# Kernel tuning notes

Hardware: AMD Instinct MI355X
Metric: run time of the kernel (lower is better)

## Reference

```python
import jax, jax.numpy as jnp
import numpy as np

H = 256
V_IN = 32000
V_OUT = 32000
T = 2048


def setup_inputs() -> dict:
    key = jax.random.key(0)
    ks = jax.random.split(key, 16)
    s = 1.0 / np.sqrt(H)
    inp = {
        "src": jax.random.randint(ks[0], (T, 1), 0, V_IN, dtype=jnp.int64 if jax.config.jax_enable_x64 else jnp.int32),
        "trg": jax.random.randint(ks[1], (T, 1), 0, V_OUT, dtype=jnp.int64 if jax.config.jax_enable_x64 else jnp.int32),
        "enc_emb": jax.random.normal(ks[2], (V_IN, H), jnp.float32),
        "enc_W_ih": jax.random.uniform(ks[3], (3 * H, H), jnp.float32, -s, s),
        "enc_W_hh": jax.random.uniform(ks[4], (3 * H, H), jnp.float32, -s, s),
        "enc_b_ih": jax.random.uniform(ks[5], (3 * H,), jnp.float32, -s, s),
        "enc_b_hh": jax.random.uniform(ks[6], (3 * H,), jnp.float32, -s, s),
        "dec_emb": jax.random.normal(ks[7], (V_OUT, H), jnp.float32),
        "dec_W_ih": jax.random.uniform(ks[8], (3 * H, H), jnp.float32, -s, s),
        "dec_W_hh": jax.random.uniform(ks[9], (3 * H, H), jnp.float32, -s, s),
        "dec_b_ih": jax.random.uniform(ks[10], (3 * H,), jnp.float32, -s, s),
        "dec_b_hh": jax.random.uniform(ks[11], (3 * H,), jnp.float32, -s, s),
        "out_W": jax.random.uniform(ks[12], (V_OUT, H), jnp.float32, -s, s),
        "out_b": jax.random.uniform(ks[13], (V_OUT,), jnp.float32, -s, s),
    }
    return inp


def _gru_step(x, h, W_ih, W_hh, b_ih, b_hh):
    # PyTorch GRU cell math. x,h: [H]
    gi = W_ih @ x + b_ih          # [3H]
    gh = W_hh @ h + b_hh          # [3H]
    i_r, i_z, i_n = jnp.split(gi, 3)
    h_r, h_z, h_n = jnp.split(gh, 3)
    r = jax.nn.sigmoid(i_r + h_r)
    z = jax.nn.sigmoid(i_z + h_z)
    n = jnp.tanh(i_n + r * h_n)
    return (1.0 - z) * n + z * h


def reference(src, trg, enc_emb, enc_W_ih, enc_W_hh, enc_b_ih, enc_b_hh,
              dec_emb, dec_W_ih, dec_W_hh, dec_b_ih, dec_b_hh, out_W, out_b):
    src_t = src[:, 0]  # [T], batch forced to 1 by .view(1,1,-1)
    trg_t = trg[:, 0]  # [T]
    h0 = jnp.zeros((H,), enc_emb.dtype)

    def step(h, toks):
        s_tok, t_tok = toks
        # encoder step
        h = _gru_step(enc_emb[s_tok], h, enc_W_ih, enc_W_hh, enc_b_ih, enc_b_hh)
        # decoder step (relu on embedding per source)
        x_d = jax.nn.relu(dec_emb[t_tok])
        h = _gru_step(x_d, h, dec_W_ih, dec_W_hh, dec_b_ih, dec_b_hh)
        logits = out_W @ h + out_b          # [V_OUT]
        return h, jax.nn.log_softmax(logits)

    _, outs = jax.lax.scan(step, h0, (src_t, trg_t))
    return outs[:, None, :]  # [T, 1, V_OUT]
```

## Files before the change

kernel.cpp:

```cpp
#include <hip/hip_runtime.h>
#include <hip/hip_bf16.h>

#define T_STEPS 2048
#define HDIM 256
#define VOUT 32000

typedef short short8 __attribute__((ext_vector_type(8)));
typedef float f32x4 __attribute__((ext_vector_type(4)));

#if defined(__has_builtin)
#if __has_builtin(__builtin_amdgcn_sdot4)
#define HAVE_SDOT4 1
#endif
#if __has_builtin(__builtin_amdgcn_mov_dpp)
#define HAVE_DPP 1
#endif
#if __has_builtin(__builtin_amdgcn_rcpf)
#define HAVE_RCP 1
#endif
#endif

__device__ __forceinline__ int dot4i8(int a, int b, int c) {
#ifdef HAVE_SDOT4
    return __builtin_amdgcn_sdot4(a, b, c, false);
#else
#pragma unroll
    for (int k = 0; k < 4; ++k) {
        int av = (a << (24 - 8 * k)) >> 24;
        int bv = (b << (24 - 8 * k)) >> 24;
        c += av * bv;
    }
    return c;
#endif
}

__device__ __forceinline__ int pairsum(int x) {
#ifdef HAVE_DPP
    return x + __builtin_amdgcn_mov_dpp(x, 0xB1, 0xF, 0xF, true);
#else
    return x + __shfl_xor(x, 1);
#endif
}

__device__ __forceinline__ float fast_rcp(float x) {
#ifdef HAVE_RCP
    return __builtin_amdgcn_rcpf(x);
#else
    return 1.0f / x;
#endif
}

__device__ __forceinline__ float fast_sigmoid(float x) {
    return fast_rcp(1.0f + __expf(-x));
}
__device__ __forceinline__ float fast_tanh(float x) {
    float ax = fabsf(x);
    float e = __expf(-2.0f * ax);
    float t = 1.0f - 2.0f * e * fast_rcp(1.0f + e);
    return copysignf(t, x);
}

__global__ void k_quant(const float* __restrict__ W, int* __restrict__ wq,
                        float* __restrict__ sc) {
    int row = blockIdx.x;
    int t = threadIdx.x;
    float4 w = ((const float4*)(W + (size_t)row * HDIM))[t];
    float m = fmaxf(fmaxf(fabsf(w.x), fabsf(w.y)), fmaxf(fabsf(w.z), fabsf(w.w)));
#pragma unroll
    for (int off = 32; off; off >>= 1) m = fmaxf(m, __shfl_xor(m, off));
    float inv = (m > 0.0f) ? 127.0f / m : 0.0f;
    float scale = (m > 0.0f) ? m * (1.0f / 127.0f) : 0.0f;
    int q0 = __float2int_rn(w.x * inv); q0 = max(-127, min(127, q0));
    int q1 = __float2int_rn(w.y * inv); q1 = max(-127, min(127, q1));
    int q2 = __float2int_rn(w.z * inv); q2 = max(-127, min(127, q2));
    int q3 = __float2int_rn(w.w * inv); q3 = max(-127, min(127, q3));
    int packed = (q0 & 255) | ((q1 & 255) << 8) | ((q2 & 255) << 16) | ((q3 & 255) << 24);
    wq[row * 64 + t] = packed;
    if (t == 0) sc[row] = scale;
}

__global__ __launch_bounds__(256) void k_cvt(const float* __restrict__ in,
                                             unsigned short* __restrict__ out, int n4) {
    int i = blockIdx.x * 256 + threadIdx.x;
    if (i < n4) {
        float4 v = ((const float4*)in)[i];
        unsigned int u[4] = {__float_as_uint(v.x), __float_as_uint(v.y),
                             __float_as_uint(v.z), __float_as_uint(v.w)};
        ushort4 o;
        o.x = (unsigned short)((u[0] + 0x7FFFu + ((u[0] >> 16) & 1)) >> 16);
        o.y = (unsigned short)((u[1] + 0x7FFFu + ((u[1] >> 16) & 1)) >> 16);
        o.z = (unsigned short)((u[2] + 0x7FFFu + ((u[2] >> 16) & 1)) >> 16);
        o.w = (unsigned short)((u[3] + 0x7FFFu + ((u[3] >> 16) & 1)) >> 16);
        ((ushort4*)out)[i] = o;
    }
}

__global__ __launch_bounds__(256) void k_gi(const int* __restrict__ toks,
                                            const float* __restrict__ emb,
                                            const float* __restrict__ W,
                                            const float* __restrict__ b,
                                            float* __restrict__ gi, int do_relu) {
    __shared__ float4 xs[64];
    int t = blockIdx.x;
    int tid = threadIdx.x;
    int tok = toks[t];
    if (tid < 64) {
        float4 x = ((const float4*)(emb + (size_t)tok * HDIM))[tid];
        if (do_relu) {
            x.x = fmaxf(x.x, 0.0f); x.y = fmaxf(x.y, 0.0f);
            x.z = fmaxf(x.z, 0.0f); x.w = fmaxf(x.w, 0.0f);
        }
        xs[tid] = x;
    }
    __syncthreads();
#pragma unroll
    for (int g = 0; g < 3; ++g) {
        int row = tid + g * 256;
        const float4* wr = (const float4*)(W + (size_t)row * HDIM);
        float acc = b[row];
#pragma unroll 16
        for (int k = 0; k < 64; ++k) {
            float4 w = wr[k];
            float4 x = xs[k];
            acc += w.x * x.x + w.y * x.y + w.z * x.z + w.w * x.w;
        }
        gi[(size_t)t * 768 + row] = acc;
    }
}

__global__ __launch_bounds__(512, 2) void k_gru(
    const int* __restrict__ wq_e, const float* __restrict__ sc_e,
    const float* __restrict__ bhh_e, const float* __restrict__ gi_e,
    const int* __restrict__ wq_d, const float* __restrict__ sc_d,
    const float* __restrict__ bhh_d, const float* __restrict__ gi_d,
    unsigned short* __restrict__ h_bf) {
    __shared__ __align__(16) int HQA[64];
    __shared__ __align__(16) int HQB[64];

    const int tid = threadIdx.x;
    const int rg = tid >> 1;
    const int c  = tid & 1;

    int we[3][32], wd[3][32];
    float se[3], sd[3], be[3], bd[3];
#pragma unroll
    for (int j = 0; j < 3; ++j) {
        const int row = rg + j * 256;
        const int4* pe = (const int4*)(wq_e + (row * 64 + c * 32));
        const int4* pd = (const int4*)(wq_d + (row * 64 + c * 32));
#pragma unroll
        for (int i = 0; i < 8; ++i) {
            int4 a = pe[i];
            we[j][4 * i + 0] = a.x; we[j][4 * i + 1] = a.y;
            we[j][4 * i + 2] = a.z; we[j][4 * i + 3] = a.w;
            int4 bq = pd[i];
            wd[j][4 * i + 0] = bq.x; wd[j][4 * i + 1] = bq.y;
            wd[j][4 * i + 2] = bq.z; wd[j][4 * i + 3] = bq.w;
        }
        se[j] = sc_e[row] * (1.0f / 127.0f);
        sd[j] = sc_d[row] * (1.0f / 127.0f);
        be[j] = bhh_e[row];
        bd[j] = bhh_d[row];
    }

    float h = 0.0f;
    if (tid < 64) HQA[tid] = 0;
    __syncthreads();

    const float* ge = gi_e + rg;
    const float* gd = gi_d + rg;
    unsigned short* hop = h_bf + rg;

    float eg0 = ge[0], eg1 = ge[256], eg2 = ge[512];

    for (int t = 0; t < T_STEPS; ++t) {
        float dg0 = gd[0], dg1 = gd[256], dg2 = gd[512];
        gd += 768;

        {
            const int4* hq4 = ((const int4*)HQA) + c * 8;
            int p0 = 0, p1 = 0, p2 = 0;
#pragma unroll
            for (int i = 0; i < 8; ++i) {
                int4 v = hq4[i];
                p0 = dot4i8(we[0][4 * i + 0], v.x, p0);
                p1 = dot4i8(we[1][4 * i + 0], v.x, p1);
                p2 = dot4i8(we[2][4 * i + 0], v.x, p2);
                p0 = dot4i8(we[0][4 * i + 1], v.y, p0);
                p1 = dot4i8(we[1][4 * i + 1], v.y, p1);
                p2 = dot4i8(we[2][4 * i + 1], v.y, p2);
                p0 = dot4i8(we[0][4 * i + 2], v.z, p0);
                p1 = dot4i8(we[1][4 * i + 2], v.z, p1);
                p2 = dot4i8(we[2][4 * i + 2], v.z, p2);
                p0 = dot4i8(we[0][4 * i + 3], v.w, p0);
                p1 = dot4i8(we[1][4 * i + 3], v.w, p1);
                p2 = dot4i8(we[2][4 * i + 3], v.w, p2);
            }
            int f0 = pairsum(p0), f1 = pairsum(p1), f2 = pairsum(p2);
            float r = fast_sigmoid(eg0 + se[0] * (float)f0 + be[0]);
            float z = fast_sigmoid(eg1 + se[1] * (float)f1 + be[1]);
            float n = fast_tanh(eg2 + r * (se[2] * (float)f2 + be[2]));
            h = (1.0f - z) * n + z * h;
            if (c == 0)
                ((signed char*)HQB)[rg] = (signed char)__float2int_rn(h * 127.0f);
        }
        __syncthreads();

        {
            const float* gen = (t < T_STEPS - 1) ? (ge + 768) : (gi_e + rg);
            eg0 = gen[0]; eg1 = gen[256]; eg2 = gen[512];
            ge = gen;
        }

        {
            const int4* hq4 = ((const int4*)HQB) + c * 8;
            int p0 = 0, p1 = 0, p2 = 0;
#pragma unroll
            for (int i = 0; i < 8; ++i) {
                int4 v = hq4[i];
                p0 = dot4i8(wd[0][4 * i + 0], v.x, p0);
                p1 = dot4i8(wd[1][4 * i + 0], v.x, p1);
                p2 = dot4i8(wd[2][4 * i + 0], v.x, p2);
                p0 = dot4i8(wd[0][4 * i + 1], v.y, p0);
                p1 = dot4i8(wd[1][4 * i + 1], v.y, p1);
                p2 = dot4i8(wd[2][4 * i + 1], v.y, p2);
                p0 = dot4i8(wd[0][4 * i + 2], v.z, p0);
                p1 = dot4i8(wd[1][4 * i + 2], v.z, p1);
                p2 = dot4i8(wd[2][4 * i + 2], v.z, p2);
                p0 = dot4i8(wd[0][4 * i + 3], v.w, p0);
                p1 = dot4i8(wd[1][4 * i + 3], v.w, p1);
                p2 = dot4i8(wd[2][4 * i + 3], v.w, p2);
            }
            int f0 = pairsum(p0), f1 = pairsum(p1), f2 = pairsum(p2);
            float r = fast_sigmoid(dg0 + sd[0] * (float)f0 + bd[0]);
            float z = fast_sigmoid(dg1 + sd[1] * (float)f1 + bd[1]);
            float n = fast_tanh(dg2 + r * (sd[2] * (float)f2 + bd[2]));
            h = (1.0f - z) * n + z * h;
            if (c == 0) {
                ((signed char*)HQA)[rg] = (signed char)__float2int_rn(h * 127.0f);
                unsigned int u = __float_as_uint(h);
                *hop = (unsigned short)((u + 0x7FFFu + ((u >> 16) & 1)) >> 16);
            }
            hop += 256;
        }
        __syncthreads();
    }
}

__global__ __launch_bounds__(256) void k_logits(const unsigned short* __restrict__ hb,
                                                const unsigned short* __restrict__ wb,
                                                const float* __restrict__ out_b,
                                                float* __restrict__ out) {
    const int vb = blockIdx.x * 64;
    const int tb = blockIdx.y * 64;
    const int w = threadIdx.x >> 6;
    const int l = threadIdx.x & 63;
    const int m = l & 15;
    const int q = l >> 4;

    const unsigned short* aptr = hb + (size_t)(tb + w * 16 + m) * HDIM + q * 8;
    const unsigned short* bptr = wb + (size_t)(vb + m) * HDIM + q * 8;

    short8 af[8];
#pragma unroll
    for (int kt = 0; kt < 8; ++kt) af[kt] = *(const short8*)(aptr + kt * 32);

    f32x4 acc[4];
#pragma unroll
    for (int nt = 0; nt < 4; ++nt)
#pragma unroll
        for (int r = 0; r < 4; ++r) acc[nt][r] = 0.0f;

#pragma unroll
    for (int nt = 0; nt < 4; ++nt) {
        const unsigned short* bp = bptr + (size_t)nt * 16 * HDIM;
#pragma unroll
        for (int kt = 0; kt < 8; ++kt) {
            short8 bf = *(const short8*)(bp + kt * 32);
            acc[nt] = __builtin_amdgcn_mfma_f32_16x16x32_bf16(af[kt], bf, acc[nt], 0, 0, 0);
        }
    }
#pragma unroll
    for (int nt = 0; nt < 4; ++nt) {
        float bias = out_b[vb + nt * 16 + m];
#pragma unroll
        for (int r = 0; r < 4; ++r) {
            out[(size_t)(tb + w * 16 + q * 4 + r) * VOUT + vb + nt * 16 + m] =
                acc[nt][r] + bias;
        }
    }
}

__global__ __launch_bounds__(256) void k_lsesub(float* __restrict__ out) {
    const int t = blockIdx.x;
    const int tid = threadIdx.x;
    float* rowp = out + (size_t)t * VOUT;
    float m = -3.0e38f, l = 0.0f;
    for (int v = tid; v < VOUT; v += 256) {
        float x = rowp[v];
        float M = fmaxf(m, x);
        l = l * __expf(m - M) + __expf(x - M);
        m = M;
    }
#pragma unroll
    for (int off = 32; off; off >>= 1) {
        float m2 = __shfl_xor(m, off);
        float l2 = __shfl_xor(l, off);
        float M = fmaxf(m, m2);
        l = l * __expf(m - M) + l2 * __expf(m2 - M);
        m = M;
    }
    __shared__ float sm[4], sl[4];
    __shared__ float s_lse;
    int lane = tid & 63, wv = tid >> 6;
    if (lane == 0) { sm[wv] = m; sl[wv] = l; }
    __syncthreads();
    if (tid == 0) {
        float M = fmaxf(fmaxf(sm[0], sm[1]), fmaxf(sm[2], sm[3]));
        float L = sl[0] * __expf(sm[0] - M) + sl[1] * __expf(sm[1] - M) +
                  sl[2] * __expf(sm[2] - M) + sl[3] * __expf(sm[3] - M);
        s_lse = M + __logf(L);
    }
    __syncthreads();
    float s = s_lse;
    float4* p4 = (float4*)rowp;
    for (int i = tid; i < VOUT / 4; i += 256) {
        float4 o = p4[i];
        o.x -= s; o.y -= s; o.z -= s; o.w -= s;
        p4[i] = o;
    }
}

extern "C" void kernel_launch(void* const* d_in, const int* in_sizes, int n_in,
                              void* d_out, int out_size, void* d_ws, size_t ws_size,
                              hipStream_t stream) {
    (void)in_sizes; (void)n_in; (void)out_size; (void)ws_size;
    const int*   src      = (const int*)d_in[0];
    const int*   trg      = (const int*)d_in[1];
    const float* enc_emb  = (const float*)d_in[2];
    const float* enc_W_ih = (const float*)d_in[3];
    const float* enc_W_hh = (const float*)d_in[4];
    const float* enc_b_ih = (const float*)d_in[5];
    const float* enc_b_hh = (const float*)d_in[6];
    const float* dec_emb  = (const float*)d_in[7];
    const float* dec_W_ih = (const float*)d_in[8];
    const float* dec_W_hh = (const float*)d_in[9];
    const float* dec_b_ih = (const float*)d_in[10];
    const float* dec_b_hh = (const float*)d_in[11];
    const float* out_W    = (const float*)d_in[12];
    const float* out_b    = (const float*)d_in[13];
    float* out = (float*)d_out;

    char* ws = (char*)d_ws;
    float* gi_e  = (float*)ws; ws += (size_t)T_STEPS * 768 * 4;
    float* gi_d  = (float*)ws; ws += (size_t)T_STEPS * 768 * 4;
    float* sc_e  = (float*)ws; ws += 768 * 4;
    float* sc_d  = (float*)ws; ws += 768 * 4;
    int*   wq_e  = (int*)ws;   ws += 768 * 64 * 4;
    int*   wq_d  = (int*)ws;   ws += 768 * 64 * 4;
    unsigned short* h_bf = (unsigned short*)ws; ws += (size_t)T_STEPS * HDIM * 2;
    unsigned short* w_bf = (unsigned short*)ws; ws += (size_t)VOUT * HDIM * 2;

    k_quant<<<768, 64, 0, stream>>>(enc_W_hh, wq_e, sc_e);
    k_quant<<<768, 64, 0, stream>>>(dec_W_hh, wq_d, sc_d);
    k_cvt<<<(VOUT * HDIM / 4 + 255) / 256, 256, 0, stream>>>(out_W, w_bf, VOUT * HDIM / 4);
    k_gi<<<T_STEPS, 256, 0, stream>>>(src, enc_emb, enc_W_ih, enc_b_ih, gi_e, 0);
    k_gi<<<T_STEPS, 256, 0, stream>>>(trg, dec_emb, dec_W_ih, dec_b_ih, gi_d, 1);
    k_gru<<<1, 512, 0, stream>>>(wq_e, sc_e, enc_b_hh, gi_e,
                                 wq_d, sc_d, dec_b_hh, gi_d, h_bf);
    k_logits<<<dim3(VOUT / 64, T_STEPS / 64), 256, 0, stream>>>(h_bf, w_bf, out_b, out);
    k_lsesub<<<T_STEPS, 256, 0, stream>>>(out);
}
```

Before: 3.783 ms.

## Split GRU recurrence across four lanes per row pair with DPP butterfly reduction

The sequential GRU kernel now assigns two hidden units to each group of four lanes, and each lane computes a quarter-K slice for both units. A two-stage DPP exchange (xor1 swap-add, then xor2) reduces the partial sums, so each step runs half as many serial dot4 operations per lane on the critical path. The r and z hidden biases are folded into the precomputed input gates, and __syncthreads is replaced with an explicit lgkmcnt wait plus s_barrier. The cost is more cross-lane shuffles and a changed register layout, held under a waves_per_eu attribute.

```diff
diff --git a/kernel.cpp b/kernel.cpp
--- a/kernel.cpp
+++ b/kernel.cpp
@@ -34,11 +34,18 @@
 #endif
 }
 
-__device__ __forceinline__ int pairsum(int x) {
+__device__ __forceinline__ int xor1_add(int keep, int send) {
 #ifdef HAVE_DPP
-    return x + __builtin_amdgcn_mov_dpp(x, 0xB1, 0xF, 0xF, true);
+    return keep + __builtin_amdgcn_mov_dpp(send, 0xB1, 0xF, 0xF, true);
 #else
-    return x + __shfl_xor(x, 1);
+    return keep + __shfl_xor(send, 1);
+#endif
+}
+__device__ __forceinline__ int xor2_sum(int x) {
+#ifdef HAVE_DPP
+    return x + __builtin_amdgcn_mov_dpp(x, 0x4E, 0xF, 0xF, true);
+#else
+    return x + __shfl_xor(x, 2);
 #endif
 }
 
@@ -49,7 +56,6 @@
     return 1.0f / x;
 #endif
 }
-
 __device__ __forceinline__ float fast_sigmoid(float x) {
     return fast_rcp(1.0f + __expf(-x));
 }
@@ -58,6 +64,10 @@
     float e = __expf(-2.0f * ax);
     float t = 1.0f - 2.0f * e * fast_rcp(1.0f + e);
     return copysignf(t, x);
+}
+
+__device__ __forceinline__ void barrier_lds() {
+    asm volatile("s_waitcnt lgkmcnt(0)\n\ts_barrier" ::: "memory");
 }
 
 __global__ void k_quant(const float* __restrict__ W, int* __restrict__ wq,
@@ -99,6 +109,7 @@
                                             const float* __restrict__ emb,
                                             const float* __restrict__ W,
                                             const float* __restrict__ b,
+                                            const float* __restrict__ bhh,
                                             float* __restrict__ gi, int do_relu) {
     __shared__ float4 xs[64];
     int t = blockIdx.x;
@@ -117,7 +128,7 @@
     for (int g = 0; g < 3; ++g) {
         int row = tid + g * 256;
         const float4* wr = (const float4*)(W + (size_t)row * HDIM);
-        float acc = b[row];
+        float acc = b[row] + ((g < 2) ? bhh[row] : 0.0f);
 #pragma unroll 16
         for (int k = 0; k < 64; ++k) {
             float4 w = wr[k];
@@ -128,7 +139,8 @@
     }
 }
 
-__global__ __launch_bounds__(512, 2) void k_gru(
+__global__ __launch_bounds__(512)
+__attribute__((amdgpu_waves_per_eu(2, 2))) void k_gru(
     const int* __restrict__ wq_e, const float* __restrict__ sc_e,
     const float* __restrict__ bhh_e, const float* __restrict__ gi_e,
     const int* __restrict__ wq_d, const float* __restrict__ sc_d,
@@ -138,38 +150,47 @@
     __shared__ __align__(16) int HQB[64];
 
     const int tid = threadIdx.x;
-    const int rg = tid >> 1;
-    const int c  = tid & 1;
-
-    int we[3][32], wd[3][32];
-    float se[3], sd[3], be[3], bd[3];
-#pragma unroll
-    for (int j = 0; j < 3; ++j) {
-        const int row = rg + j * 256;
-        const int4* pe = (const int4*)(wq_e + (row * 64 + c * 32));
-        const int4* pd = (const int4*)(wq_d + (row * 64 + c * 32));
-#pragma unroll
-        for (int i = 0; i < 8; ++i) {
-            int4 a = pe[i];
-            we[j][4 * i + 0] = a.x; we[j][4 * i + 1] = a.y;
-            we[j][4 * i + 2] = a.z; we[j][4 * i + 3] = a.w;
-            int4 bq = pd[i];
-            wd[j][4 * i + 0] = bq.x; wd[j][4 * i + 1] = bq.y;
-            wd[j][4 * i + 2] = bq.z; wd[j][4 * i + 3] = bq.w;
-        }
-        se[j] = sc_e[row] * (1.0f / 127.0f);
-        sd[j] = sc_d[row] * (1.0f / 127.0f);
-        be[j] = bhh_e[row];
-        bd[j] = bhh_d[row];
-    }
+    const int q  = tid >> 2;
+    const int c  = tid & 3;
+    const int el = c & 1;
+    const int e  = 2 * q + el;
+    const bool wr = (c & 2) == 0;
+
+    int we[6][16], wd[6][16];
+#pragma unroll
+    for (int eo = 0; eo < 2; ++eo) {
+#pragma unroll
+        for (int g = 0; g < 3; ++g) {
+            const int row = 2 * q + eo + 256 * g;
+            const int4* pe = (const int4*)(wq_e + (row * 64 + c * 16));
+            const int4* pd = (const int4*)(wq_d + (row * 64 + c * 16));
+#pragma unroll
+            for (int i = 0; i < 4; ++i) {
+                int4 a = pe[i];
+                we[eo * 3 + g][4 * i + 0] = a.x; we[eo * 3 + g][4 * i + 1] = a.y;
+                we[eo * 3 + g][4 * i + 2] = a.z; we[eo * 3 + g][4 * i + 3] = a.w;
+                int4 bq = pd[i];
+                wd[eo * 3 + g][4 * i + 0] = bq.x; wd[eo * 3 + g][4 * i + 1] = bq.y;
+                wd[eo * 3 + g][4 * i + 2] = bq.z; wd[eo * 3 + g][4 * i + 3] = bq.w;
+            }
+        }
+    }
+    float se0 = sc_e[e] * (1.0f / 127.0f);
+    float se1 = sc_e[e + 256] * (1.0f / 127.0f);
+    float se2 = sc_e[e + 512] * (1.0f / 127.0f);
+    float sd0 = sc_d[e] * (1.0f / 127.0f);
+    float sd1 = sc_d[e + 256] * (1.0f / 127.0f);
+    float sd2 = sc_d[e + 512] * (1.0f / 127.0f);
+    float be2 = bhh_e[e + 512];
+    float bd2 = bhh_d[e + 512];
 
     float h = 0.0f;
     if (tid < 64) HQA[tid] = 0;
     __syncthreads();
 
-    const float* ge = gi_e + rg;
-    const float* gd = gi_d + rg;
-    unsigned short* hop = h_bf + rg;
+    const float* ge = gi_e + e;
+    const float* gd = gi_d + e;
+    unsigned short* hop = h_bf + e;
 
     float eg0 = ge[0], eg1 = ge[256], eg2 = ge[512];
 
@@ -178,72 +199,68 @@
         gd += 768;
 
         {
-            const int4* hq4 = ((const int4*)HQA) + c * 8;
-            int p0 = 0, p1 = 0, p2 = 0;
-#pragma unroll
-            for (int i = 0; i < 8; ++i) {
+            const int4* hq4 = ((const int4*)HQA) + c * 4;
+            int p[6] = {0, 0, 0, 0, 0, 0};
+#pragma unroll
+            for (int i = 0; i < 4; ++i) {
                 int4 v = hq4[i];
-                p0 = dot4i8(we[0][4 * i + 0], v.x, p0);
-                p1 = dot4i8(we[1][4 * i + 0], v.x, p1);
-                p2 = dot4i8(we[2][4 * i + 0], v.x, p2);
-                p0 = dot4i8(we[0][4 * i + 1], v.y, p0);
-                p1 = dot4i8(we[1][4 * i + 1], v.y, p1);
-                p2 = dot4i8(we[2][4 * i + 1], v.y, p2);
-                p0 = dot4i8(we[0][4 * i + 2], v.z, p0);
-                p1 = dot4i8(we[1][4 * i + 2], v.z, p1);
-                p2 = dot4i8(we[2][4 * i + 2], v.z, p2);
-                p0 = dot4i8(we[0][4 * i + 3], v.w, p0);
-                p1 = dot4i8(we[1][4 * i + 3], v.w, p1);
-                p2 = dot4i8(we[2][4 * i + 3], v.w, p2);
+#pragma unroll
+                for (int j = 0; j < 6; ++j) {
+                    p[j] = dot4i8(we[j][4 * i + 0], v.x, p[j]);
+                    p[j] = dot4i8(we[j][4 * i + 1], v.y, p[j]);
+                    p[j] = dot4i8(we[j][4 * i + 2], v.z, p[j]);
+                    p[j] = dot4i8(we[j][4 * i + 3], v.w, p[j]);
+                }
             }
-            int f0 = pairsum(p0), f1 = pairsum(p1), f2 = pairsum(p2);
-            float r = fast_sigmoid(eg0 + se[0] * (float)f0 + be[0]);
-            float z = fast_sigmoid(eg1 + se[1] * (float)f1 + be[1]);
-            float n = fast_tanh(eg2 + r * (se[2] * (float)f2 + be[2]));
+            int f0 = xor1_add(el ? p[3] : p[0], el ? p[0] : p[3]);
+            int f1 = xor1_add(el ? p[4] : p[1], el ? p[1] : p[4]);
+            int f2 = xor1_add(el ? p[5] : p[2], el ? p[2] : p[5]);
+            f0 = xor2_sum(f0); f1 = xor2_sum(f1); f2 = xor2_sum(f2);
+            float r = fast_sigmoid(eg0 + se0 * (float)f0);
+            float z = fast_sigmoid(eg1 + se1 * (float)f1);
+            float n = fast_tanh(eg2 + r * (se2 * (float)f2 + be2));
             h = (1.0f - z) * n + z * h;
-            if (c == 0)
-                ((signed char*)HQB)[rg] = (signed char)__float2int_rn(h * 127.0f);
-        }
-        __syncthreads();
+            if (wr)
+                ((signed char*)HQB)[e] = (signed char)__float2int_rn(h * 127.0f);
+        }
+        barrier_lds();
 
         {
-            const float* gen = (t < T_STEPS - 1) ? (ge + 768) : (gi_e + rg);
+            const float* gen = (t < T_STEPS - 1) ? (ge + 768) : (gi_e + e);
             eg0 = gen[0]; eg1 = gen[256]; eg2 = gen[512];
             ge = gen;
         }
 
         {
-            const int4* hq4 = ((const int4*)HQB) + c * 8;
-            int p0 = 0, p1 = 0, p2 = 0;
-#pragma unroll
-            for (int i = 0; i < 8; ++i) {
+            const int4* hq4 = ((const int4*)HQB) + c * 4;
+            int p[6] = {0, 0, 0, 0, 0, 0};
+#pragma unroll
+            for (int i = 0; i < 4; ++i) {
                 int4 v = hq4[i];
-                p0 = dot4i8(wd[0][4 * i + 0], v.x, p0);
-                p1 = dot4i8(wd[1][4 * i + 0], v.x, p1);
-                p2 = dot4i8(wd[2][4 * i + 0], v.x, p2);
-                p0 = dot4i8(wd[0][4 * i + 1], v.y, p0);
-                p1 = dot4i8(wd[1][4 * i + 1], v.y, p1);
-                p2 = dot4i8(wd[2][4 * i + 1], v.y, p2);
-                p0 = dot4i8(wd[0][4 * i + 2], v.z, p0);
-                p1 = dot4i8(wd[1][4 * i + 2], v.z, p1);
-                p2 = dot4i8(wd[2][4 * i + 2], v.z, p2);
-                p0 = dot4i8(wd[0][4 * i + 3], v.w, p0);
-                p1 = dot4i8(wd[1][4 * i + 3], v.w, p1);
-                p2 = dot4i8(wd[2][4 * i + 3], v.w, p2);
+#pragma unroll
+                for (int j = 0; j < 6; ++j) {
+                    p[j] = dot4i8(wd[j][4 * i + 0], v.x, p[j]);
+                    p[j] = dot4i8(wd[j][4 * i + 1], v.y, p[j]);
+                    p[j] = dot4i8(wd[j][4 * i + 2], v.z, p[j]);
+                    p[j] = dot4i8(wd[j][4 * i + 3], v.w, p[j]);
+                }
             }
-            int f0 = pairsum(p0), f1 = pairsum(p1), f2 = pairsum(p2);
-            float r = fast_sigmoid(dg0 + sd[0] * (float)f0 + bd[0]);
-            float z = fast_sigmoid(dg1 + sd[1] * (float)f1 + bd[1]);
-            float n = fast_tanh(dg2 + r * (sd[2] * (float)f2 + bd[2]));
+            int f0 = xor1_add(el ? p[3] : p[0], el ? p[0] : p[3]);
+            int f1 = xor1_add(el ? p[4] : p[1], el ? p[1] : p[4]);
+            int f2 = xor1_add(el ? p[5] : p[2], el ? p[2] : p[5]);
+            f0 = xor2_sum(f0); f1 = xor2_sum(f1); f2 = xor2_sum(f2);
+            float r = fast_sigmoid(dg0 + sd0 * (float)f0);
+            float z = fast_sigmoid(dg1 + sd1 * (float)f1);
+            float n = fast_tanh(dg2 + r * (sd2 * (float)f2 + bd2));
             h = (1.0f - z) * n + z * h;
-            if (c == 0) {
-                ((signed char*)HQA)[rg] = (signed char)__float2int_rn(h * 127.0f);
+            if (wr) {
+                ((signed char*)HQA)[e] = (signed char)__float2int_rn(h * 127.0f);
                 unsigned int u = __float_as_uint(h);
                 *hop = (unsigned short)((u + 0x7FFFu + ((u >> 16) & 1)) >> 16);
             }
             hop += 256;
         }
-        __syncthreads();
+        barrier_lds();
     }
 }
 
@@ -364,8 +381,8 @@
     k_quant<<<768, 64, 0, stream>>>(enc_W_hh, wq_e, sc_e);
     k_quant<<<768, 64, 0, stream>>>(dec_W_hh, wq_d, sc_d);
     k_cvt<<<(VOUT * HDIM / 4 + 255) / 256, 256, 0, stream>>>(out_W, w_bf, VOUT * HDIM / 4);
-    k_gi<<<T_STEPS, 256, 0, stream>>>(src, enc_emb, enc_W_ih, enc_b_ih, gi_e, 0);
-    k_gi<<<T_STEPS, 256, 0, stream>>>(trg, dec_emb, dec_W_ih, dec_b_ih, gi_d, 1);
+    k_gi<<<T_STEPS, 256, 0, stream>>>(src, enc_emb, enc_W_ih, enc_b_ih, enc_b_hh, gi_e, 0);
+    k_gi<<<T_STEPS, 256, 0, stream>>>(trg, dec_emb, dec_W_ih, dec_b_ih, dec_b_hh, gi_d, 1);
     k_gru<<<1, 512, 0, stream>>>(wq_e, sc_e, enc_b_hh, gi_e,
                                  wq_d, sc_d, dec_b_hh, gi_d, h_bf);
     k_logits<<<dim3(VOUT / 64, T_STEPS / 64), 256, 0, stream>>>(h_bf, w_bf, out_b, out);
```

After: 3.771 ms. Within noise of the previous version (-0.3%).
